# Optimization experiments

Hardware: AMD Instinct MI355X
Metric: run time of the kernel (lower is better)

## Reference

```python
import jax, jax.numpy as jnp
import numpy as np

HEAD_SIZE = 64  # n_embds // n_heads = 1024 // 16

def setup_inputs() -> dict:
    key = jax.random.key(0)
    k0, k1, k2, k3 = jax.random.split(key, 4)
    B, S, D, H = 4, 4096, 1024, HEAD_SIZE
    scale = 1.0 / np.sqrt(D)
    return {
        "decoder_input": jax.random.normal(k0, (B, S, D), dtype=jnp.float32),
        "Wq": jax.random.normal(k1, (D, H), dtype=jnp.float32) * scale,
        "Wk": jax.random.normal(k2, (D, H), dtype=jnp.float32) * scale,
        "Wv": jax.random.normal(k3, (D, H), dtype=jnp.float32) * scale,
    }

def reference(decoder_input, Wq, Wk, Wv):
    # q,k,v: [B,S,H]; Linear(bias=False) == x @ W
    q = decoder_input @ Wq
    k = decoder_input @ Wk
    v = decoder_input @ Wv
    head_size = k.shape[2]
    # scores: [B,S,S] -- full materialization, as in the original
    scores = jnp.einsum('bqh,bkh->bqk', q, k) / jnp.sqrt(jnp.float32(head_size))
    S = scores.shape[1]
    causal = jnp.tril(jnp.ones((S, S), dtype=bool))  # lower-triangular mask
    masked = jnp.where(causal, scores, -jnp.inf)
    attn = jax.nn.softmax(masked, axis=2)
    # dropout_rate = 0.0 -> identity
    return jnp.einsum('bqk,bkh->bqh', attn, v)
```

## Files before the change

kernel.cpp:

```cpp
#include <hip/hip_runtime.h>
#include <hip/hip_bf16.h>
#include <math.h>

typedef __bf16 bf16_t;
typedef __bf16 bf16x8 __attribute__((ext_vector_type(8)));
typedef float f32x4 __attribute__((ext_vector_type(4)));

constexpr int SS = 4096;
constexpr int DD = 1024;
constexpr int HH = 64;

#if __has_builtin(__builtin_amdgcn_exp2f)
#define EXP2F __builtin_amdgcn_exp2f
#else
#define EXP2F exp2f
#endif

static __device__ __forceinline__ f32x4 mfma16(bf16x8 a, bf16x8 b, f32x4 c) {
  return __builtin_amdgcn_mfma_f32_16x16x32_bf16(a, b, c, 0, 0, 0);
}

__global__ __launch_bounds__(256) void prep_w(const float* __restrict__ wq,
                                              const float* __restrict__ wk,
                                              const float* __restrict__ wv,
                                              bf16_t* __restrict__ wt) {
  __shared__ float ls[64 * 68];
  int tid = threadIdx.x;
  int sel = blockIdx.x >> 4, kb = blockIdx.x & 15, k0 = kb * 64;
  const float* src = (sel == 0) ? wq : ((sel == 1) ? wk : wv);
  int bn = sel * 64;
#pragma unroll
  for (int i = 0; i < 4; ++i) {
    int e = tid + i * 256;
    int r = e >> 4, c4 = (e & 15) * 4;
    *(float4*)&ls[r * 68 + c4] = *(const float4*)(src + (size_t)(k0 + r) * 64 + c4);
  }
  __syncthreads();
#pragma unroll
  for (int j = 0; j < 2; ++j) {
    int e = tid + j * 256;
    int n = e >> 3, kg = e & 7;
    bf16x8 v;
#pragma unroll
    for (int t = 0; t < 8; ++t) v[t] = (bf16_t)ls[(kg * 8 + t) * 68 + n];
    *(bf16x8*)(wt + (size_t)(bn + n) * 1024 + k0 + kg * 8) = v;
  }
}

__global__ __launch_bounds__(256) void gemm_qkv(const float* __restrict__ x,
                                                const bf16_t* __restrict__ wt,
                                                bf16_t* __restrict__ qo,
                                                bf16_t* __restrict__ ko,
                                                bf16_t* __restrict__ vto) {
  __shared__ bf16_t xs[2][32 * 64];
  __shared__ bf16_t wsh[2][192 * 64];
  int tid = threadIdx.x;
  int wave = tid >> 6, lane = tid & 63, quad = lane >> 4, ml = lane & 15;
  int m0 = blockIdx.x * 32;
  int mtile = wave >> 1;
  int nt0 = (wave & 1) * 6;

  f32x4 acc[6];
#pragma unroll
  for (int i = 0; i < 6; ++i) acc[i] = (f32x4){0.f, 0.f, 0.f, 0.f};

  int xrow = tid >> 3, xseg = tid & 7;
  float4 xr[2];
  bf16x8 wr[6];

  auto load_g = [&](int k0) {
    const float* p = x + (size_t)(m0 + xrow) * DD + k0 + xseg * 8;
    xr[0] = *(const float4*)p;
    xr[1] = *(const float4*)(p + 4);
#pragma unroll
    for (int i = 0; i < 6; ++i) {
      int c = tid + i * 256;
      int r = c >> 3, cc = c & 7;
      wr[i] = *(const bf16x8*)(wt + (size_t)r * DD + k0 + cc * 8);
    }
  };
  auto store_lds = [&](int bf) {
    bf16x8 v0;
    v0[0] = (bf16_t)xr[0].x; v0[1] = (bf16_t)xr[0].y;
    v0[2] = (bf16_t)xr[0].z; v0[3] = (bf16_t)xr[0].w;
    v0[4] = (bf16_t)xr[1].x; v0[5] = (bf16_t)xr[1].y;
    v0[6] = (bf16_t)xr[1].z; v0[7] = (bf16_t)xr[1].w;
    int cc0 = xseg ^ (xrow & 7);
    *(bf16x8*)&xs[bf][xrow * 64 + cc0 * 8] = v0;
#pragma unroll
    for (int i = 0; i < 6; ++i) {
      int c = tid + i * 256;
      int r = c >> 3, cc = c & 7;
      *(bf16x8*)&wsh[bf][r * 64 + ((cc ^ (r & 7)) * 8)] = wr[i];
    }
  };

  load_g(0);
  store_lds(0);
  load_g(64);
  __syncthreads();
  for (int it = 0; it < 16; ++it) {
    int bf = it & 1;
#pragma unroll
    for (int s = 0; s < 2; ++s) {
      int rchunk = ((s * 4 + quad) ^ (ml & 7)) * 8;
      bf16x8 a = *(const bf16x8*)&xs[bf][(mtile * 16 + ml) * 64 + rchunk];
#pragma unroll
      for (int i = 0; i < 6; ++i) {
        bf16x8 bfr = *(const bf16x8*)&wsh[bf][((nt0 + i) * 16 + ml) * 64 + rchunk];
        acc[i] = mfma16(a, bfr, acc[i]);
      }
    }
    if (it < 15) {
      store_lds(1 - bf);
      if (it < 14) load_g((it + 2) * 64);
      __syncthreads();
    }
  }

  int b = m0 >> 12;
  int sr = m0 & 4095;
  const float QSCALE = 0.18033688011112042f;
  bf16_t* vls = (bf16_t*)wsh;
#pragma unroll
  for (int i = 0; i < 6; ++i) {
    int col = (wave & 1) * 96 + i * 16 + ml;
#pragma unroll
    for (int r = 0; r < 4; ++r) {
      int lrow = mtile * 16 + quad * 4 + r;
      size_t grow = (size_t)b * SS + sr + lrow;
      if (col < 64) qo[grow * HH + col] = (bf16_t)(acc[i][r] * QSCALE);
      else if (col < 128) ko[grow * HH + (col - 64)] = (bf16_t)(acc[i][r]);
      else vls[(col - 128) * 40 + lrow] = (bf16_t)(acc[i][r]);
    }
  }
  __syncthreads();
  {
    int h = tid >> 2, sg = tid & 3;
    *(bf16x8*)(vto + ((size_t)b * HH + h) * SS + sr + sg * 8) =
        *(const bf16x8*)&vls[h * 40 + sg * 8];
  }
}

__global__ __launch_bounds__(256) void attn_partial(const bf16_t* __restrict__ qg,
                                                    const bf16_t* __restrict__ kg,
                                                    const bf16_t* __restrict__ vg,
                                                    float* __restrict__ partO,
                                                    float* __restrict__ lb,
                                                    float* __restrict__ out) {
  __shared__ bf16_t Kl[64 * 64];
  __shared__ bf16_t Vl[64 * 64];
  __shared__ bf16_t Pl[4][16 * 64];
  int tid = threadIdx.x;
  int wave = tid >> 6, lane = tid & 63, quad = lane >> 4, ml = lane & 15;

  int bid = blockIdx.x;
  int b = bid & 3;
  int j = 343 - (bid >> 2);
  int jt, ch, nch;
  if (j < 8)        { jt = j;                   ch = 0;            nch = 1; }
  else if (j < 24)  { jt = 8  + ((j - 8) >> 1); ch = (j - 8) & 1;  nch = 2; }
  else if (j < 88)  { jt = 16 + ((j - 24) >> 2); ch = (j - 24) & 3; nch = 4; }
  else              { jt = 32 + ((j - 88) >> 3); ch = (j - 88) & 7; nch = 8; }
  int L = (jt + nch) / nch;
  int c0 = ch * L;
  int c1 = c0 + L; if (c1 > jt + 1) c1 = jt + 1;
  int len = c1 - c0;
  bool direct = (nch == 1);
  int slot = b * 336 + (j - 8);
  int q0 = jt * 64;

  const bf16_t* qb = qg + (size_t)b * SS * HH;
  const bf16_t* kb = kg + (size_t)b * SS * HH;
  const bf16_t* vb = vg + (size_t)b * HH * SS;

  int qrow = q0 + wave * 16 + ml;
  bf16x8 aq0 = *(const bf16x8*)(qb + (size_t)qrow * HH + quad * 8);
  bf16x8 aq1 = *(const bf16x8*)(qb + (size_t)qrow * HH + 32 + quad * 8);

  bf16x8 kreg[2], vreg[2];
  int srl = tid >> 3, scc = tid & 7;
  auto load_kv = [&](int kt) {
#pragma unroll
    for (int i = 0; i < 2; ++i) {
      int r = srl + i * 32;
      kreg[i] = *(const bf16x8*)(kb + (size_t)(kt * 64 + r) * HH + scc * 8);
      vreg[i] = *(const bf16x8*)(vb + (size_t)r * SS + kt * 64 + scc * 8);
    }
  };
  auto store_kv = [&]() {
#pragma unroll
    for (int i = 0; i < 2; ++i) {
      int r = srl + i * 32;
      int off = r * 64 + ((scc ^ (r & 7)) * 8);
      *(bf16x8*)&Kl[off] = kreg[i];
      *(bf16x8*)&Vl[off] = vreg[i];
    }
  };

  f32x4 oa[4];
#pragma unroll
  for (int i = 0; i < 4; ++i) oa[i] = (f32x4){0.f, 0.f, 0.f, 0.f};
  float lr[4] = {0.f, 0.f, 0.f, 0.f};

  load_kv(c0);

  for (int i = 0; i < len; ++i) {
    int kt = c0 + i;
    __syncthreads();
    store_kv();
    __syncthreads();
    if (i + 1 < len) load_kv(kt + 1);

    f32x4 sa[4];
#pragma unroll
    for (int nt = 0; nt < 4; ++nt) sa[nt] = (f32x4){0.f, 0.f, 0.f, 0.f};
#pragma unroll
    for (int s = 0; s < 2; ++s) {
      bf16x8 a = s ? aq1 : aq0;
      int rchunk = ((s * 4 + quad) ^ (ml & 7)) * 8;
#pragma unroll
      for (int nt = 0; nt < 4; ++nt) {
        bf16x8 bfr = *(const bf16x8*)&Kl[(nt * 16 + ml) * 64 + rchunk];
        sa[nt] = mfma16(a, bfr, sa[nt]);
      }
    }

    if (kt == jt) {
#pragma unroll
      for (int nt = 0; nt < 4; ++nt) {
        int key = kt * 64 + nt * 16 + ml;
#pragma unroll
        for (int r = 0; r < 4; ++r) {
          int qr = q0 + wave * 16 + quad * 4 + r;
          if (key > qr) sa[nt][r] = -3.38953139e38f;
        }
      }
    }

#pragma unroll
    for (int r = 0; r < 4; ++r) {
      float p0 = EXP2F(sa[0][r]);
      float p1 = EXP2F(sa[1][r]);
      float p2 = EXP2F(sa[2][r]);
      float p3 = EXP2F(sa[3][r]);
      sa[0][r] = p0; sa[1][r] = p1; sa[2][r] = p2; sa[3][r] = p3;
      lr[r] += (p0 + p1) + (p2 + p3);
    }

#pragma unroll
    for (int nt = 0; nt < 4; ++nt) {
#pragma unroll
      for (int r = 0; r < 4; ++r) {
        int row = quad * 4 + r;
        int cc = nt * 2 + (ml >> 3);
        Pl[wave][row * 64 + ((cc ^ (row & 7)) * 8) + (ml & 7)] = (bf16_t)sa[nt][r];
      }
    }
#pragma unroll
    for (int s = 0; s < 2; ++s) {
      int rchunk = ((s * 4 + quad) ^ (ml & 7)) * 8;
      bf16x8 pa = *(const bf16x8*)&Pl[wave][ml * 64 + rchunk];
#pragma unroll
      for (int ht = 0; ht < 4; ++ht) {
        bf16x8 bv = *(const bf16x8*)&Vl[(ht * 16 + ml) * 64 + rchunk];
        oa[ht] = mfma16(pa, bv, oa[ht]);
      }
    }
  }

#pragma unroll
  for (int r = 0; r < 4; ++r) {
    float t = lr[r];
    t += __shfl_xor(t, 1);
    t += __shfl_xor(t, 2);
    t += __shfl_xor(t, 4);
    t += __shfl_xor(t, 8);
    lr[r] = t;
  }

  if (direct) {
#pragma unroll
    for (int r = 0; r < 4; ++r) {
      float inv = 1.0f / lr[r];
      int row = q0 + wave * 16 + quad * 4 + r;
#pragma unroll
      for (int ht = 0; ht < 4; ++ht)
        out[((size_t)b * SS + row) * HH + ht * 16 + ml] = oa[ht][r] * inv;
    }
  } else {
    float* po = partO + (size_t)slot * 4096;
#pragma unroll
    for (int r = 0; r < 4; ++r) {
      int row = wave * 16 + quad * 4 + r;
#pragma unroll
      for (int ht = 0; ht < 4; ++ht)
        po[row * 64 + ht * 16 + ml] = oa[ht][r];
      if (ml == 0) lb[slot * 64 + row] = lr[r];
    }
  }
}

__global__ __launch_bounds__(256) void combine(const float* __restrict__ partO,
                                               const float* __restrict__ lb,
                                               float* __restrict__ out) {
  int bid = blockIdx.x;
  int b = bid / 56;
  int jt = 8 + (bid - b * 56);
  int nch, jbase;
  if (jt < 16)      { nch = 2; jbase = 8 + 2 * (jt - 8); }
  else if (jt < 32) { nch = 4; jbase = 24 + 4 * (jt - 16); }
  else              { nch = 8; jbase = 88 + 8 * (jt - 32); }
  int base = b * 336 + (jbase - 8);
  int tid = threadIdx.x;
  int row = tid >> 2, cb = tid & 3;

  float l = 0.f;
  f32x4 o[4];
#pragma unroll
  for (int jj = 0; jj < 4; ++jj) o[jj] = (f32x4){0.f, 0.f, 0.f, 0.f};
  for (int c = 0; c < nch; ++c) {
    l += lb[(base + c) * 64 + row];
    const f32x4* p = (const f32x4*)(partO + (size_t)(base + c) * 4096 + row * 64 + cb * 16);
#pragma unroll
    for (int jj = 0; jj < 4; ++jj) o[jj] += p[jj];
  }
  float inv = 1.0f / l;
  f32x4* op = (f32x4*)(out + (((size_t)b * SS) + jt * 64 + row) * HH + cb * 16);
#pragma unroll
  for (int jj = 0; jj < 4; ++jj) op[jj] = o[jj] * inv;
}

extern "C" void kernel_launch(void* const* d_in, const int* in_sizes, int n_in,
                              void* d_out, int out_size, void* d_ws, size_t ws_size,
                              hipStream_t stream) {
  const float* x  = (const float*)d_in[0];
  const float* wq = (const float*)d_in[1];
  const float* wk = (const float*)d_in[2];
  const float* wv = (const float*)d_in[3];
  float* out = (float*)d_out;

  char* wsb = (char*)d_ws;
  bf16_t* wt  = (bf16_t*)wsb;
  bf16_t* q   = (bf16_t*)(wsb + 524288);
  bf16_t* k   = (bf16_t*)(wsb + 2621440);
  bf16_t* vt  = (bf16_t*)(wsb + 4718592);
  float*  po  = (float*)(wsb + 6815744);
  float*  lb  = (float*)(wsb + 28835840);

  prep_w<<<48, 256, 0, stream>>>(wq, wk, wv, wt);
  gemm_qkv<<<512, 256, 0, stream>>>(x, wt, q, k, vt);
  attn_partial<<<1376, 256, 0, stream>>>(q, k, vt, po, lb, out);
  combine<<<224, 256, 0, stream>>>(po, lb, out);
}
```

Measured before the change: 140.2 us.

## Fuse split-KV combine into attention kernel via last-block atomic counter

Removes the separate combine kernel launch. Each split-chunk block writes its partial output, fences, and bumps a per-tile atomic counter. The last block to finish reduces all partials, reusing its own accumulators from registers, and writes the normalized output. This saves one kernel launch and the reread of one partial, but adds an atomic, fences and extra __syncthreads to every split block, plus a serial reduction tail on the last block.

```diff
diff --git a/kernel.cpp b/kernel.cpp
--- a/kernel.cpp
+++ b/kernel.cpp
@@ -23,9 +23,11 @@
 __global__ __launch_bounds__(256) void prep_w(const float* __restrict__ wq,
                                               const float* __restrict__ wk,
                                               const float* __restrict__ wv,
-                                              bf16_t* __restrict__ wt) {
+                                              bf16_t* __restrict__ wt,
+                                              int* __restrict__ cnt) {
   __shared__ float ls[64 * 68];
   int tid = threadIdx.x;
+  if (blockIdx.x == 0 && tid < 224) cnt[tid] = 0;
   int sel = blockIdx.x >> 4, kb = blockIdx.x & 15, k0 = kb * 64;
   const float* src = (sel == 0) ? wq : ((sel == 1) ? wk : wv);
   int bn = sel * 64;
@@ -147,10 +149,12 @@
                                                     const bf16_t* __restrict__ vg,
                                                     float* __restrict__ partO,
                                                     float* __restrict__ lb,
+                                                    int* __restrict__ cnt,
                                                     float* __restrict__ out) {
   __shared__ bf16_t Kl[64 * 64];
   __shared__ bf16_t Vl[64 * 64];
   __shared__ bf16_t Pl[4][16 * 64];
+  __shared__ int lastf;
   int tid = threadIdx.x;
   int wave = tid >> 6, lane = tid & 63, quad = lane >> 4, ml = lane & 15;
 
@@ -298,37 +302,36 @@
         po[row * 64 + ht * 16 + ml] = oa[ht][r];
       if (ml == 0) lb[slot * 64 + row] = lr[r];
     }
-  }
-}
-
-__global__ __launch_bounds__(256) void combine(const float* __restrict__ partO,
-                                               const float* __restrict__ lb,
-                                               float* __restrict__ out) {
-  int bid = blockIdx.x;
-  int b = bid / 56;
-  int jt = 8 + (bid - b * 56);
-  int nch, jbase;
-  if (jt < 16)      { nch = 2; jbase = 8 + 2 * (jt - 8); }
-  else if (jt < 32) { nch = 4; jbase = 24 + 4 * (jt - 16); }
-  else              { nch = 8; jbase = 88 + 8 * (jt - 32); }
-  int base = b * 336 + (jbase - 8);
-  int tid = threadIdx.x;
-  int row = tid >> 2, cb = tid & 3;
-
-  float l = 0.f;
-  f32x4 o[4];
-#pragma unroll
-  for (int jj = 0; jj < 4; ++jj) o[jj] = (f32x4){0.f, 0.f, 0.f, 0.f};
-  for (int c = 0; c < nch; ++c) {
-    l += lb[(base + c) * 64 + row];
-    const f32x4* p = (const f32x4*)(partO + (size_t)(base + c) * 4096 + row * 64 + cb * 16);
-#pragma unroll
-    for (int jj = 0; jj < 4; ++jj) o[jj] += p[jj];
-  }
-  float inv = 1.0f / l;
-  f32x4* op = (f32x4*)(out + (((size_t)b * SS) + jt * 64 + row) * HH + cb * 16);
-#pragma unroll
-  for (int jj = 0; jj < 4; ++jj) op[jj] = o[jj] * inv;
+    __threadfence();
+    __syncthreads();
+    int jobid = b * 56 + (jt - 8);
+    if (tid == 0)
+      lastf = (atomicAdd(&cnt[jobid], 1) == nch - 1);
+    __syncthreads();
+    if (lastf) {
+      __threadfence();
+      int s0 = slot - ch;
+#pragma unroll
+      for (int r = 0; r < 4; ++r) {
+        int row = wave * 16 + quad * 4 + r;
+        float lsum = lr[r];
+        float o0 = oa[0][r], o1 = oa[1][r], o2 = oa[2][r], o3 = oa[3][r];
+        for (int c = 0; c < nch; ++c) {
+          if (c == ch) continue;
+          const float* pc = partO + (size_t)(s0 + c) * 4096 + row * 64;
+          lsum += lb[(s0 + c) * 64 + row];
+          o0 += pc[ml];      o1 += pc[16 + ml];
+          o2 += pc[32 + ml]; o3 += pc[48 + ml];
+        }
+        float inv = 1.0f / lsum;
+        size_t orow = ((size_t)b * SS + q0 + row) * HH;
+        out[orow + ml]      = o0 * inv;
+        out[orow + 16 + ml] = o1 * inv;
+        out[orow + 32 + ml] = o2 * inv;
+        out[orow + 48 + ml] = o3 * inv;
+      }
+    }
+  }
 }
 
 extern "C" void kernel_launch(void* const* d_in, const int* in_sizes, int n_in,
@@ -347,9 +350,9 @@
   bf16_t* vt  = (bf16_t*)(wsb + 4718592);
   float*  po  = (float*)(wsb + 6815744);
   float*  lb  = (float*)(wsb + 28835840);
-
-  prep_w<<<48, 256, 0, stream>>>(wq, wk, wv, wt);
+  int*    cnt = (int*)(wsb + 29360128);
+
+  prep_w<<<48, 256, 0, stream>>>(wq, wk, wv, wt, cnt);
   gemm_qkv<<<512, 256, 0, stream>>>(x, wt, q, k, vt);
-  attn_partial<<<1376, 256, 0, stream>>>(q, k, vt, po, lb, out);
-  combine<<<224, 256, 0, stream>>>(po, lb, out);
-}
+  attn_partial<<<1376, 256, 0, stream>>>(q, k, vt, po, lb, cnt, out);
+}
```

Result: slower. 330.9 us (+136.0%).
